# Optimization experiments

Hardware: AMD Instinct MI355X
Metric: run time of the kernel (lower is better)

## Reference

```python
import jax, jax.numpy as jnp
import numpy as np

P, H_IMG, W_IMG, D, NH, NL, DM, DO = 16, 64, 1024, 512, 8, 6, 2048, 512
B, C = 64, 3
PH, PW = H_IMG // P, W_IMG // P
NPATCH = PH * PW
L = NPATCH + 1
EPS = 1e-5


def _ln(x, s, b):
    m = jnp.mean(x, axis=-1, keepdims=True)
    v = jnp.var(x, axis=-1, keepdims=True)
    return (x - m) * jax.lax.rsqrt(v + EPS) * s + b


def setup_inputs() -> dict:
    key = jax.random.key(0)
    ks = iter(jax.random.split(key, 40))
    n = lambda shape, scale=0.02: jax.random.normal(next(ks), shape, dtype=jnp.float32) * scale
    inp = {
        "pixel_values": jax.random.normal(next(ks), (B, C, H_IMG, W_IMG), dtype=jnp.float32),
        "patch_w": n((C * P * P, D)), "patch_b": jnp.zeros((D,), jnp.float32),
        "row_emb": n((H_IMG // P + 1, D // 2)), "col_emb": n((W_IMG // P + 1, D // 2)),
        "cls": n((1, D)),
        "ln1_s": jnp.ones((NL, D), jnp.float32), "ln1_b": jnp.zeros((NL, D), jnp.float32),
        "qkv_w": n((NL, D, 3 * D)), "qkv_b": jnp.zeros((NL, 3 * D), jnp.float32),
        "out_w": n((NL, D, D)), "out_b": jnp.zeros((NL, D), jnp.float32),
        "ln2_s": jnp.ones((NL, D), jnp.float32), "ln2_b": jnp.zeros((NL, D), jnp.float32),
        "mlp_w1": n((NL, D, DM)), "mlp_b1": jnp.zeros((NL, DM), jnp.float32),
        "mlp_w2": n((NL, DM, D)), "mlp_b2": jnp.zeros((NL, D), jnp.float32),
        "lnf_s": jnp.ones((D,), jnp.float32), "lnf_b": jnp.zeros((D,), jnp.float32),
        "br_w1": n((D, 2 * D)), "br_b1": jnp.zeros((2 * D,), jnp.float32),
        "br_w2": n((2 * D, DO)), "br_b2": jnp.zeros((DO,), jnp.float32),
        "br_ln_s": jnp.ones((DO,), jnp.float32), "br_ln_b": jnp.zeros((DO,), jnp.float32),
    }
    return inp


def reference(pixel_values, patch_w, patch_b, row_emb, col_emb, cls,
              ln1_s, ln1_b, qkv_w, qkv_b, out_w, out_b, ln2_s, ln2_b,
              mlp_w1, mlp_b1, mlp_w2, mlp_b2, lnf_s, lnf_b,
              br_w1, br_b1, br_w2, br_b2, br_ln_s, br_ln_b):
    # --- patchify (vectorized over batch): [B,C,H,W] -> [B, ph*pw, C*P*P]
    patches = pixel_values.reshape(B, C, PH, P, PW, P)
    patches = patches.transpose(0, 2, 4, 1, 3, 5).reshape(B, NPATCH, C * P * P)
    # --- 2D factored positional embedding: [ph*pw, D]
    pos = jnp.concatenate([
        jnp.broadcast_to(row_emb[:PH, None, :], (PH, PW, D // 2)),
        jnp.broadcast_to(col_emb[None, :PW, :], (PH, PW, D // 2)),
    ], axis=-1).reshape(NPATCH, D)
    emb = patches @ patch_w + patch_b + pos  # [B, NPATCH, D]
    x = jnp.concatenate([jnp.broadcast_to(cls[None], (B, 1, D)), emb], axis=1)  # [B, L, D]
    # All images have equal length; the block-diagonal -inf mask over the packed
    # sequence is exactly batched per-image self-attention (same math).
    dh = D // NH
    scale = 1.0 / np.sqrt(dh)
    for l in range(NL):
        n1 = _ln(x, ln1_s[l], ln1_b[l])
        qkv = n1 @ qkv_w[l] + qkv_b[l]  # [B, L, 3D]
        q, k, v = jnp.split(qkv, 3, axis=-1)
        q = q.reshape(B, L, NH, dh).transpose(0, 2, 1, 3)
        k = k.reshape(B, L, NH, dh).transpose(0, 2, 1, 3)
        v = v.reshape(B, L, NH, dh).transpose(0, 2, 1, 3)
        scores = jnp.einsum('bhqd,bhkd->bhqk', q, k) * scale
        attn = jax.nn.softmax(scores, axis=-1)
        o = jnp.einsum('bhqk,bhkd->bhqd', attn, v)
        o = o.transpose(0, 2, 1, 3).reshape(B, L, D)
        x = x + (o @ out_w[l] + out_b[l])
        n2 = _ln(x, ln2_s[l], ln2_b[l])
        h = jax.nn.gelu(n2 @ mlp_w1[l] + mlp_b1[l], approximate=False)
        x = x + (h @ mlp_w2[l] + mlp_b2[l])
    x = _ln(x, lnf_s, lnf_b)  # encoded, [B, L, D]
    vis_mask = jnp.ones((B, L), dtype=jnp.int32)
    # BridgeMLP
    h = jax.nn.gelu(x @ br_w1 + br_b1, approximate=False) @ br_w2 + br_b2
    out = _ln(h, br_ln_s, br_ln_b)
    return out, vis_mask
```

## Files before the change

kernel.cpp:

```cpp
#include <hip/hip_runtime.h>
#include <cstdint>

typedef unsigned short u16;
typedef unsigned int   u32;

typedef short bf16x8 __attribute__((ext_vector_type(8)));
typedef float f32x4  __attribute__((ext_vector_type(4)));

#define MFMA(a,b,c) __builtin_amdgcn_mfma_f32_16x16x32_bf16(a,b,c,0,0,0)

#define GLD16(g, s) __builtin_amdgcn_global_load_lds(                      \
    (const __attribute__((address_space(1))) void*)(g),                    \
    (__attribute__((address_space(3))) void*)(s), 16, 0, 0)

__device__ __forceinline__ u16 f2b(float f) {
  u32 u = __float_as_uint(f);
  u += 0x7FFFu + ((u >> 16) & 1u);
  return (u16)(u >> 16);
}

__global__ __launch_bounds__(256) void transp_k(const float* __restrict__ W,
                                                u16* __restrict__ WT, int K, int N) {
  __shared__ float t[32][33];
  int tx = threadIdx.x & 31, ty = threadIdx.x >> 5;
  long bo = (long)blockIdx.z * K * N;
  int n0 = blockIdx.x * 32, k0 = blockIdx.y * 32;
  const float* Wp = W + bo;
  u16* Tp = WT + bo;
#pragma unroll
  for (int i = 0; i < 32; i += 8)
    t[ty + i][tx] = Wp[(long)(k0 + ty + i) * N + n0 + tx];
  __syncthreads();
#pragma unroll
  for (int i = 0; i < 32; i += 8)
    Tp[(long)(n0 + ty + i) * K + k0 + tx] = f2b(t[tx][ty + i]);
}

__global__ __launch_bounds__(256) void patchify_k(const float* __restrict__ pix,
                                                  u16* __restrict__ patA) {
  int idx = blockIdx.x * 256 + threadIdx.x;
  int x = idx & 1023;
  int y = (idx >> 10) & 63;
  int c = (idx >> 16) % 3;
  int b = idx / 196608;
  int p  = ((y >> 4) << 6) | (x >> 4);
  int ci = (c << 8) | ((y & 15) << 4) | (x & 15);
  patA[(long)(b * 256 + p) * 768 + ci] = f2b(pix[idx]);
}

__global__ __launch_bounds__(256) void cls_k(const float* __restrict__ cls,
                                             float* __restrict__ xF) {
  int i = blockIdx.x * 256 + threadIdx.x;
  int b = i >> 9, n = i & 511;
  xF[(long)(b * 257) * 512 + n] = cls[n];
}

template <int OUT>
__global__ __launch_bounds__(256) void ln_k(const float* __restrict__ x,
                                            const float* __restrict__ gm,
                                            const float* __restrict__ bt,
                                            u16* __restrict__ outB,
                                            float* __restrict__ outF) {
  int row = blockIdx.x * 4 + (threadIdx.x >> 6);
  int l = threadIdx.x & 63;
  const float* xr = x + (long)row * 512 + l * 8;
  float v[8];
  *(float4*)(v)     = *(const float4*)(xr);
  *(float4*)(v + 4) = *(const float4*)(xr + 4);
  float s = 0.f, s2 = 0.f;
#pragma unroll
  for (int j = 0; j < 8; ++j) { s += v[j]; s2 += v[j] * v[j]; }
#pragma unroll
  for (int xm = 1; xm < 64; xm <<= 1) {
    s  += __shfl_xor(s, xm);
    s2 += __shfl_xor(s2, xm);
  }
  float m   = s * (1.f / 512.f);
  float var = fmaxf(s2 * (1.f / 512.f) - m * m, 0.f);
  float rs  = rsqrtf(var + 1e-5f);
  if (OUT == 0) {
    u16 o8[8];
#pragma unroll
    for (int j = 0; j < 8; ++j)
      o8[j] = f2b((v[j] - m) * rs * gm[l * 8 + j] + bt[l * 8 + j]);
    *(uint4*)&outB[(long)row * 512 + l * 8] = *(const uint4*)o8;
  } else {
    float o8[8];
#pragma unroll
    for (int j = 0; j < 8; ++j)
      o8[j] = (v[j] - m) * rs * gm[l * 8 + j] + bt[l * 8 + j];
    float* op = outF + (long)row * 512 + l * 8;
    *(float4*)(op)     = *(const float4*)(o8);
    *(float4*)(op + 4) = *(const float4*)(o8 + 4);
  }
}

template <int EPI>
__global__ __launch_bounds__(256) void gemm_k(
    const u16* __restrict__ A, const u16* __restrict__ Bt,
    const float* __restrict__ bias, const float* __restrict__ res,
    float* __restrict__ outF, u16* __restrict__ outB,
    int N, int K, int Mreal,
    const float* __restrict__ aux1, const float* __restrict__ aux2) {
  __shared__ u16 As[128 * 32];
  __shared__ u16 Bs[128 * 32];
  int tid = threadIdx.x, w = tid >> 6, l = tid & 63, g = l >> 4, c = l & 15;
  int mt = blockIdx.y, nt = blockIdx.x;
  int wr = (w >> 1) * 64, wc = (w & 1) * 64;
  f32x4 zero = {0.f, 0.f, 0.f, 0.f};
  f32x4 acc[4][4];
#pragma unroll
  for (int m = 0; m < 4; ++m)
#pragma unroll
    for (int n = 0; n < 4; ++n) acc[m][n] = zero;

  int c0 = w * 128 + l;
  int c1 = c0 + 64;
  long gOff0 = (long)(c0 >> 2) * K + (c0 & 3) * 8;
  long gOff1 = (long)(c1 >> 2) * K + (c1 & 3) * 8;
  u16* lA0 = &As[(w * 128) * 8];
  u16* lA1 = &As[(w * 128 + 64) * 8];
  u16* lB0 = &Bs[(w * 128) * 8];
  u16* lB1 = &Bs[(w * 128 + 64) * 8];
  const u16* Ab = A + (long)(mt * 128) * K;
  const u16* Bb = Bt + (long)(nt * 128) * K;

  for (int k0 = 0; k0 < K; k0 += 32) {
    __syncthreads();
    GLD16(Ab + gOff0 + k0, lA0);
    GLD16(Ab + gOff1 + k0, lA1);
    GLD16(Bb + gOff0 + k0, lB0);
    GLD16(Bb + gOff1 + k0, lB1);
    __syncthreads();
    bf16x8 af[4], bfr[4];
#pragma unroll
    for (int m = 0; m < 4; ++m)
      af[m] = *(const bf16x8*)&As[(wr + m * 16 + c) * 32 + g * 8];
#pragma unroll
    for (int n = 0; n < 4; ++n)
      bfr[n] = *(const bf16x8*)&Bs[(wc + n * 16 + c) * 32 + g * 8];
#pragma unroll
    for (int m = 0; m < 4; ++m)
#pragma unroll
      for (int n = 0; n < 4; ++n)
        acc[m][n] = MFMA(af[m], bfr[n], acc[m][n]);
  }

  long Nl = N;
#pragma unroll
  for (int m = 0; m < 4; ++m) {
    int rbase = mt * 128 + wr + m * 16 + g * 4;
#pragma unroll
    for (int n = 0; n < 4; ++n) {
      int col = nt * 128 + wc + n * 16 + c;
      float bv = bias[col];
#pragma unroll
      for (int q = 0; q < 4; ++q) {
        int row = rbase + q;
        if (row >= Mreal) continue;
        float v = acc[m][n][q] + bv;
        if (EPI == 0) {
          int pb = row >> 8, p = row & 255;
          float pos = (col < 256) ? aux1[(p >> 6) * 256 + col]
                                  : aux2[(p & 63) * 256 + col - 256];
          outF[(long)(pb * 257 + 1 + p) * 512 + col] = v + pos;
        } else if (EPI == 1) {
          outB[(long)row * Nl + col] = f2b(v);
        } else if (EPI == 2) {
          outF[(long)row * Nl + col] = res[(long)row * Nl + col] + v;
        } else if (EPI == 3) {
          float gv = v * 0.5f * (1.0f + erff(v * 0.70710678118f));
          outB[(long)row * Nl + col] = f2b(gv);
        } else {
          outF[(long)row * Nl + col] = v;
        }
      }
    }
  }
}

__global__ __launch_bounds__(256) void attn_scores_k(const u16* __restrict__ qkv,
                                                     u16* __restrict__ P) {
  __shared__ u16 Kl[272 * 72];
  int bx = blockIdx.x;
  int bh = bx / 5, qb = bx % 5;
  int b = bh >> 3, h = bh & 7;
  int tid = threadIdx.x, w = tid >> 6, l = tid & 63, g = l >> 4, c = l & 15;
  long qkvbase = ((long)b * 257) * 1536 + h * 64;

  for (int ch = tid; ch < 2056; ch += 256) {
    int r = ch >> 3, ko = (ch & 7) * 8;
    *(uint4*)&Kl[r * 72 + ko] =
        *(const uint4*)&qkv[qkvbase + 512 + (long)r * 1536 + ko];
  }
  __syncthreads();

  int q0 = qb * 64 + w * 16;
  bf16x8 aq0 = *(const bf16x8*)&qkv[qkvbase + (long)(q0 + c) * 1536 + g * 8];
  bf16x8 aq1 = *(const bf16x8*)&qkv[qkvbase + (long)(q0 + c) * 1536 + 32 + g * 8];

  f32x4 sreg[17];
#pragma unroll
  for (int t = 0; t < 17; ++t) {
    f32x4 a = {0.f, 0.f, 0.f, 0.f};
    a = MFMA(aq0, *(const bf16x8*)&Kl[(t * 16 + c) * 72 + g * 8], a);
    a = MFMA(aq1, *(const bf16x8*)&Kl[(t * 16 + c) * 72 + 32 + g * 8], a);
    sreg[t] = a;
  }

  float mrow[4] = {-1e30f, -1e30f, -1e30f, -1e30f};
#pragma unroll
  for (int t = 0; t < 17; ++t) {
    bool valid = (t * 16 + c) < 257;
#pragma unroll
    for (int q = 0; q < 4; ++q) {
      float v = valid ? sreg[t][q] * 0.125f : -1e30f;
      sreg[t][q] = v;
      mrow[q] = fmaxf(mrow[q], v);
    }
  }
#pragma unroll
  for (int xm = 1; xm < 16; xm <<= 1)
#pragma unroll
    for (int q = 0; q < 4; ++q)
      mrow[q] = fmaxf(mrow[q], __shfl_xor(mrow[q], xm));

  float ssum[4] = {0.f, 0.f, 0.f, 0.f};
#pragma unroll
  for (int t = 0; t < 17; ++t)
#pragma unroll
    for (int q = 0; q < 4; ++q) {
      float e = __expf(sreg[t][q] - mrow[q]);
      sreg[t][q] = e;
      ssum[q] += e;
    }
#pragma unroll
  for (int xm = 1; xm < 16; xm <<= 1)
#pragma unroll
    for (int q = 0; q < 4; ++q) ssum[q] += __shfl_xor(ssum[q], xm);

#pragma unroll
  for (int q = 0; q < 4; ++q) {
    int qg = q0 + g * 4 + q;
    if (qg < 257) {
      float rs = 1.0f / ssum[q];
      long pb = ((long)bh * 272 + qg) * 288;
#pragma unroll
      for (int t = 0; t < 17; ++t)
        P[pb + t * 16 + c] = f2b(sreg[t][q] * rs);
    }
  }
}

__global__ __launch_bounds__(256) void attn_pv_k(const u16* __restrict__ qkv,
                                                 const u16* __restrict__ P,
                                                 u16* __restrict__ o) {
  __shared__ u16 Vt[64 * 296];
  int bx = blockIdx.x;
  int bh = bx / 5, qb = bx % 5;
  int b = bh >> 3, h = bh & 7;
  int tid = threadIdx.x, w = tid >> 6, l = tid & 63, g = l >> 4, c = l & 15;
  long vbase = ((long)b * 257) * 1536 + h * 64 + 1024;

  for (int e = tid; e < 16448; e += 256) {
    int r = e >> 6, d = e & 63;
    Vt[d * 296 + r] = qkv[vbase + (long)r * 1536 + d];
  }
  for (int e = tid; e < 64 * 39; e += 256) {
    int d = e / 39, k = 257 + (e - d * 39);
    Vt[d * 296 + k] = 0;
  }
  __syncthreads();

  int q0 = qb * 64 + w * 16;
  int arow = q0 + c;
  if (arow > 271) arow = 271;
  long pbase = ((long)bh * 272 + arow) * 288;

  f32x4 zero = {0.f, 0.f, 0.f, 0.f};
  f32x4 oacc[4] = {zero, zero, zero, zero};
#pragma unroll
  for (int ch = 0; ch < 9; ++ch) {
    bf16x8 ap = *(const bf16x8*)&P[pbase + ch * 32 + g * 8];
#pragma unroll
    for (int dt = 0; dt < 4; ++dt) {
      bf16x8 bv = *(const bf16x8*)&Vt[(dt * 16 + c) * 296 + ch * 32 + g * 8];
      oacc[dt] = MFMA(ap, bv, oacc[dt]);
    }
  }
#pragma unroll
  for (int dt = 0; dt < 4; ++dt)
#pragma unroll
    for (int q = 0; q < 4; ++q) {
      int qg = q0 + g * 4 + q;
      if (qg < 257)
        o[((long)b * 257 + qg) * 512 + h * 64 + dt * 16 + c] = f2b(oacc[dt][q]);
    }
}

__global__ __launch_bounds__(256) void mask_k(float* __restrict__ out) {
  int i = blockIdx.x * 256 + threadIdx.x;
  if (i < 16448) out[8421376 + i] = 1.0f;
}

extern "C" void kernel_launch(void* const* d_in, const int* in_sizes, int n_in,
                              void* d_out, int out_size, void* d_ws, size_t ws_size,
                              hipStream_t stream) {
  const float* pix     = (const float*)d_in[0];
  const float* patch_w = (const float*)d_in[1];
  const float* patch_b = (const float*)d_in[2];
  const float* row_emb = (const float*)d_in[3];
  const float* col_emb = (const float*)d_in[4];
  const float* clsv    = (const float*)d_in[5];
  const float* ln1_s   = (const float*)d_in[6];
  const float* ln1_b   = (const float*)d_in[7];
  const float* qkv_w   = (const float*)d_in[8];
  const float* qkv_b   = (const float*)d_in[9];
  const float* out_w   = (const float*)d_in[10];
  const float* out_b   = (const float*)d_in[11];
  const float* ln2_s   = (const float*)d_in[12];
  const float* ln2_b   = (const float*)d_in[13];
  const float* mlp_w1  = (const float*)d_in[14];
  const float* mlp_b1  = (const float*)d_in[15];
  const float* mlp_w2  = (const float*)d_in[16];
  const float* mlp_b2  = (const float*)d_in[17];
  const float* lnf_s   = (const float*)d_in[18];
  const float* lnf_b   = (const float*)d_in[19];
  const float* br_w1   = (const float*)d_in[20];
  const float* br_b1   = (const float*)d_in[21];
  const float* br_w2   = (const float*)d_in[22];
  const float* br_b2   = (const float*)d_in[23];
  const float* brln_s  = (const float*)d_in[24];
  const float* brln_b  = (const float*)d_in[25];
  (void)in_sizes; (void)n_in; (void)out_size; (void)ws_size;

  char* ws = (char*)d_ws;
  float* xF   = (float*)(ws);
  u16*   nB   = (u16*)(ws + 34078720ull);
  u16*   qkvB = (u16*)(ws + 51118080ull);
  u16*   oB   = (u16*)(ws + 102236160ull);
  u16*   hB   = (u16*)(ws + 119275520ull);
  u16*   wt   = (u16*)(ws + 199491584ull);
  u16* wtPatch = wt;
  u16* wtQkv   = wtPatch + 393216;
  u16* wtOut   = wtQkv + 4718592;
  u16* wtM1    = wtOut + 1572864;
  u16* wtM2    = wtM1 + 6291456;
  u16* wtB1    = wtM2 + 6291456;
  u16* wtB2    = wtB1 + 524288;
  u16*   patA = hB;
  u16*   Pbuf = hB;
  float* brF  = (float*)qkvB;

  dim3 blk(256);
  transp_k<<<dim3(16, 24, 1), blk, 0, stream>>>(patch_w, wtPatch, 768, 512);
  transp_k<<<dim3(48, 16, 6), blk, 0, stream>>>(qkv_w, wtQkv, 512, 1536);
  transp_k<<<dim3(16, 16, 6), blk, 0, stream>>>(out_w, wtOut, 512, 512);
  transp_k<<<dim3(64, 16, 6), blk, 0, stream>>>(mlp_w1, wtM1, 512, 2048);
  transp_k<<<dim3(16, 64, 6), blk, 0, stream>>>(mlp_w2, wtM2, 2048, 512);
  transp_k<<<dim3(32, 16, 1), blk, 0, stream>>>(br_w1, wtB1, 512, 1024);
  transp_k<<<dim3(16, 32, 1), blk, 0, stream>>>(br_w2, wtB2, 1024, 512);

  patchify_k<<<49152, blk, 0, stream>>>(pix, patA);
  cls_k<<<128, blk, 0, stream>>>(clsv, xF);
  gemm_k<0><<<dim3(4, 128), blk, 0, stream>>>(patA, wtPatch, patch_b, nullptr,
                                              xF, nullptr, 512, 768, 16384,
                                              row_emb, col_emb);

  for (int l = 0; l < 6; ++l) {
    ln_k<0><<<4112, blk, 0, stream>>>(xF, ln1_s + l * 512, ln1_b + l * 512, nB, nullptr);
    gemm_k<1><<<dim3(12, 129), blk, 0, stream>>>(nB, wtQkv + (size_t)l * 786432,
                                                 qkv_b + l * 1536, nullptr,
                                                 nullptr, qkvB, 1536, 512, 16448,
                                                 nullptr, nullptr);
    attn_scores_k<<<2560, blk, 0, stream>>>(qkvB, Pbuf);
    attn_pv_k<<<2560, blk, 0, stream>>>(qkvB, Pbuf, oB);
    gemm_k<2><<<dim3(4, 129), blk, 0, stream>>>(oB, wtOut + (size_t)l * 262144,
                                                out_b + l * 512, xF, xF, nullptr,
                                                512, 512, 16448, nullptr, nullptr);
    ln_k<0><<<4112, blk, 0, stream>>>(xF, ln2_s + l * 512, ln2_b + l * 512, nB, nullptr);
    gemm_k<3><<<dim3(16, 129), blk, 0, stream>>>(nB, wtM1 + (size_t)l * 1048576,
                                                 mlp_b1 + l * 2048, nullptr,
                                                 nullptr, hB, 2048, 512, 16448,
                                                 nullptr, nullptr);
    gemm_k<2><<<dim3(4, 129), blk, 0, stream>>>(hB, wtM2 + (size_t)l * 1048576,
                                                mlp_b2 + l * 512, xF, xF, nullptr,
                                                512, 2048, 16448, nullptr, nullptr);
  }

  ln_k<0><<<4112, blk, 0, stream>>>(xF, lnf_s, lnf_b, nB, nullptr);
  gemm_k<3><<<dim3(8, 129), blk, 0, stream>>>(nB, wtB1, br_b1, nullptr, nullptr,
                                              hB, 1024, 512, 16448, nullptr, nullptr);
  gemm_k<4><<<dim3(4, 129), blk, 0, stream>>>(hB, wtB2, br_b2, nullptr, brF,
                                              nullptr, 512, 1024, 16448, nullptr,
                                              nullptr);
  ln_k<1><<<4112, blk, 0, stream>>>(brF, brln_s, brln_b, nullptr, (float*)d_out);
  mask_k<<<65, blk, 0, stream>>>((float*)d_out);
}
```

Before: 2.490 ms.

## Double-buffer GEMM LDS tiles and swizzle workgroups across XCDs

The GEMM kernel now stages K-tiles into two LDS buffers, so the global-to-LDS load for the next tile is issued before the MFMAs on the current one. This replaces two barriers per iteration with one. Launches switch to a 1D grid with an XCD-aware remap, so consecutive tiles sharing A rows land on the same XCD for better L2 reuse. The cost is double the LDS use, which may lower occupancy, and the remap must cover the grid exactly.

```diff
diff --git a/kernel.cpp b/kernel.cpp
--- a/kernel.cpp
+++ b/kernel.cpp
@@ -100,12 +100,18 @@
     const u16* __restrict__ A, const u16* __restrict__ Bt,
     const float* __restrict__ bias, const float* __restrict__ res,
     float* __restrict__ outF, u16* __restrict__ outB,
-    int N, int K, int Mreal,
+    int N, int K, int Mreal, int nx,
     const float* __restrict__ aux1, const float* __restrict__ aux2) {
-  __shared__ u16 As[128 * 32];
-  __shared__ u16 Bs[128 * 32];
+  __shared__ u16 As[2][4096];
+  __shared__ u16 Bs[2][4096];
   int tid = threadIdx.x, w = tid >> 6, l = tid & 63, g = l >> 4, c = l & 15;
-  int mt = blockIdx.y, nt = blockIdx.x;
+
+  int nwg = gridDim.x, bid = blockIdx.x;
+  int qd = nwg >> 3, r = nwg & 7;
+  int xcd = bid & 7, idx = bid >> 3;
+  int swz = (xcd < r ? xcd * (qd + 1) : r * (qd + 1) + (xcd - r) * qd) + idx;
+  int mt = swz / nx, nt = swz - mt * nx;
+
   int wr = (w >> 1) * 64, wc = (w & 1) * 64;
   f32x4 zero = {0.f, 0.f, 0.f, 0.f};
   f32x4 acc[4][4];
@@ -115,36 +121,42 @@
     for (int n = 0; n < 4; ++n) acc[m][n] = zero;
 
   int c0 = w * 128 + l;
-  int c1 = c0 + 64;
   long gOff0 = (long)(c0 >> 2) * K + (c0 & 3) * 8;
-  long gOff1 = (long)(c1 >> 2) * K + (c1 & 3) * 8;
-  u16* lA0 = &As[(w * 128) * 8];
-  u16* lA1 = &As[(w * 128 + 64) * 8];
-  u16* lB0 = &Bs[(w * 128) * 8];
-  u16* lB1 = &Bs[(w * 128 + 64) * 8];
+  long gOff1 = (long)((c0 + 64) >> 2) * K + ((c0 + 64) & 3) * 8;
   const u16* Ab = A + (long)(mt * 128) * K;
   const u16* Bb = Bt + (long)(nt * 128) * K;
-
-  for (int k0 = 0; k0 < K; k0 += 32) {
-    __syncthreads();
-    GLD16(Ab + gOff0 + k0, lA0);
-    GLD16(Ab + gOff1 + k0, lA1);
-    GLD16(Bb + gOff0 + k0, lB0);
-    GLD16(Bb + gOff1 + k0, lB1);
-    __syncthreads();
+  int wb = w * 1024;
+
+#define STAGE(buf, kk)                                                     \
+  do {                                                                     \
+    GLD16(Ab + gOff0 + (kk), &As[buf][wb]);                                \
+    GLD16(Ab + gOff1 + (kk), &As[buf][wb + 512]);                          \
+    GLD16(Bb + gOff0 + (kk), &Bs[buf][wb]);                                \
+    GLD16(Bb + gOff1 + (kk), &Bs[buf][wb + 512]);                          \
+  } while (0)
+
+  int NTk = K >> 5;
+  STAGE(0, 0);
+  __syncthreads();
+  int cur = 0;
+  for (int t = 0; t < NTk; ++t) {
+    if (t + 1 < NTk) STAGE(cur ^ 1, (t + 1) << 5);
     bf16x8 af[4], bfr[4];
 #pragma unroll
     for (int m = 0; m < 4; ++m)
-      af[m] = *(const bf16x8*)&As[(wr + m * 16 + c) * 32 + g * 8];
+      af[m] = *(const bf16x8*)&As[cur][(wr + m * 16 + c) * 32 + g * 8];
 #pragma unroll
     for (int n = 0; n < 4; ++n)
-      bfr[n] = *(const bf16x8*)&Bs[(wc + n * 16 + c) * 32 + g * 8];
+      bfr[n] = *(const bf16x8*)&Bs[cur][(wc + n * 16 + c) * 32 + g * 8];
 #pragma unroll
     for (int m = 0; m < 4; ++m)
 #pragma unroll
       for (int n = 0; n < 4; ++n)
         acc[m][n] = MFMA(af[m], bfr[n], acc[m][n]);
-  }
+    __syncthreads();
+    cur ^= 1;
+  }
+#undef STAGE
 
   long Nl = N;
 #pragma unroll
@@ -363,37 +375,37 @@
 
   patchify_k<<<49152, blk, 0, stream>>>(pix, patA);
   cls_k<<<128, blk, 0, stream>>>(clsv, xF);
-  gemm_k<0><<<dim3(4, 128), blk, 0, stream>>>(patA, wtPatch, patch_b, nullptr,
-                                              xF, nullptr, 512, 768, 16384,
-                                              row_emb, col_emb);
+  gemm_k<0><<<512, blk, 0, stream>>>(patA, wtPatch, patch_b, nullptr,
+                                     xF, nullptr, 512, 768, 16384, 4,
+                                     row_emb, col_emb);
 
   for (int l = 0; l < 6; ++l) {
     ln_k<0><<<4112, blk, 0, stream>>>(xF, ln1_s + l * 512, ln1_b + l * 512, nB, nullptr);
-    gemm_k<1><<<dim3(12, 129), blk, 0, stream>>>(nB, wtQkv + (size_t)l * 786432,
-                                                 qkv_b + l * 1536, nullptr,
-                                                 nullptr, qkvB, 1536, 512, 16448,
-                                                 nullptr, nullptr);
+    gemm_k<1><<<1548, blk, 0, stream>>>(nB, wtQkv + (size_t)l * 786432,
+                                        qkv_b + l * 1536, nullptr,
+                                        nullptr, qkvB, 1536, 512, 16448, 12,
+                                        nullptr, nullptr);
     attn_scores_k<<<2560, blk, 0, stream>>>(qkvB, Pbuf);
     attn_pv_k<<<2560, blk, 0, stream>>>(qkvB, Pbuf, oB);
-    gemm_k<2><<<dim3(4, 129), blk, 0, stream>>>(oB, wtOut + (size_t)l * 262144,
-                                                out_b + l * 512, xF, xF, nullptr,
-                                                512, 512, 16448, nullptr, nullptr);
+    gemm_k<2><<<516, blk, 0, stream>>>(oB, wtOut + (size_t)l * 262144,
+                                       out_b + l * 512, xF, xF, nullptr,
+                                       512, 512, 16448, 4, nullptr, nullptr);
     ln_k<0><<<4112, blk, 0, stream>>>(xF, ln2_s + l * 512, ln2_b + l * 512, nB, nullptr);
-    gemm_k<3><<<dim3(16, 129), blk, 0, stream>>>(nB, wtM1 + (size_t)l * 1048576,
-                                                 mlp_b1 + l * 2048, nullptr,
-                                                 nullptr, hB, 2048, 512, 16448,
-                                                 nullptr, nullptr);
-    gemm_k<2><<<dim3(4, 129), blk, 0, stream>>>(hB, wtM2 + (size_t)l * 1048576,
-                                                mlp_b2 + l * 512, xF, xF, nullptr,
-                                                512, 2048, 16448, nullptr, nullptr);
+    gemm_k<3><<<2064, blk, 0, stream>>>(nB, wtM1 + (size_t)l * 1048576,
+                                        mlp_b1 + l * 2048, nullptr,
+                                        nullptr, hB, 2048, 512, 16448, 16,
+                                        nullptr, nullptr);
+    gemm_k<2><<<516, blk, 0, stream>>>(hB, wtM2 + (size_t)l * 1048576,
+                                       mlp_b2 + l * 512, xF, xF, nullptr,
+                                       512, 2048, 16448, 4, nullptr, nullptr);
   }
 
   ln_k<0><<<4112, blk, 0, stream>>>(xF, lnf_s, lnf_b, nB, nullptr);
-  gemm_k<3><<<dim3(8, 129), blk, 0, stream>>>(nB, wtB1, br_b1, nullptr, nullptr,
-                                              hB, 1024, 512, 16448, nullptr, nullptr);
-  gemm_k<4><<<dim3(4, 129), blk, 0, stream>>>(hB, wtB2, br_b2, nullptr, brF,
-                                              nullptr, 512, 1024, 16448, nullptr,
-                                              nullptr);
+  gemm_k<3><<<1032, blk, 0, stream>>>(nB, wtB1, br_b1, nullptr, nullptr,
+                                      hB, 1024, 512, 16448, 8, nullptr, nullptr);
+  gemm_k<4><<<516, blk, 0, stream>>>(hB, wtB2, br_b2, nullptr, brF,
+                                     nullptr, 512, 1024, 16448, 4, nullptr,
+                                     nullptr);
   ln_k<1><<<4112, blk, 0, stream>>>(brF, brln_s, brln_b, nullptr, (float*)d_out);
   mask_k<<<65, blk, 0, stream>>>((float*)d_out);
 }
```

New measurement: 2.336 ms. 1.07x faster.
